# Kernel tuning notes

Measured on AMD Instinct MI355X. Metric: run time of the kernel, lower is better.

The kernel has to match this reference:

```python
import jax, jax.numpy as jnp
import numpy as np

EMBED = 1024
TOKLEN = 100
NLAYERS = 24
TOKDIM = 256
MLP = int(EMBED * 0.125)  # 128, hardcoded mlp_ratio=0.125
SEQ, BATCH = 4097, 8  # 4096 patch tokens + 1 cls token


def setup_inputs() -> dict:
    key = jax.random.key(0)
    ks = jax.random.split(key, 8)
    s = 0.02  # kaiming-like small init scale
    return {
        "x": jax.random.normal(ks[0], (SEQ, BATCH, EMBED), jnp.float32),
        "layer": 3,
        "A": jax.random.normal(ks[1], (1, TOKLEN, EMBED), jnp.float32) * s,
        "B": jax.random.normal(ks[2], (NLAYERS, EMBED, TOKDIM), jnp.float32) * s,
        "Wd": jax.random.normal(ks[3], (MLP, TOKDIM), jnp.float32) * s,
        "bd": jnp.zeros((MLP,), jnp.float32),
        "Wu": jax.random.normal(ks[4], (EMBED, MLP), jnp.float32) * s,
        "bu": jnp.zeros((EMBED,), jnp.float32),
        "Wt": jax.random.normal(ks[5], (EMBED, EMBED), jnp.float32) * s,
        "bt": jnp.zeros((EMBED,), jnp.float32),
        "Wf": jax.random.normal(ks[6], (EMBED, EMBED), jnp.float32) * s,
        "bf": jnp.zeros((EMBED,), jnp.float32),
        "scale": jnp.asarray(0.001, jnp.float32),
    }


def reference(x, layer, A, B, Wd, bd, Wu, bu, Wt, bt, Wf, bf, scale):
    # batch_first=False, has_cls_token=True, evp_feature=None (module defaults)
    cls_tok, body = x[:1], x[1:]              # [1,b,c], [n,b,c]
    # get_tokens(layer): tokens = A[0] @ up(gelu(down(B[layer])))
    Bl = B[layer]                              # [c, token_dim]
    fB = jax.nn.gelu(Bl @ Wd.T + bd, approximate=False) @ Wu.T + bu  # [c, c]
    tokens = A[0] @ fB                         # [m, c]
    # forward_delta_feat: cross-attention to the m=100 learned tokens
    attn = jax.nn.softmax(
        jnp.einsum("nbc,mc->nbm", body, tokens) * (EMBED ** -0.5), axis=-1
    )                                          # [n, b, m]
    tfeat = tokens @ Wt.T + bt                 # mlp_token2feat, [m, c]
    delta = jnp.einsum("nbm,mc->nbc", attn, tfeat)
    delta = (delta + body) @ Wf.T + bf         # mlp_delta_f
    out = body + delta * scale                 # scaled residual fuse
    return jnp.concatenate([cls_tok, out], axis=0)
```

## Files before the change

### kernel.cpp

```cpp
#include <hip/hip_runtime.h>
#include <stdint.h>

#define EMBED 1024
#define TOKLEN 100
#define TOKDIM 256
#define MLPD 128
#define KEXT 1152

typedef float f32x4 __attribute__((ext_vector_type(4)));
typedef __bf16 bf16x8 __attribute__((ext_vector_type(8)));

__device__ __forceinline__ unsigned short f2bf(float f) {
  unsigned int u = __float_as_uint(f);
  u += 0x7fffu + ((u >> 16) & 1);
  return (unsigned short)(u >> 16);
}
__device__ __forceinline__ float bf2f(unsigned short h) {
  return __uint_as_float(((unsigned int)h) << 16);
}
__device__ __forceinline__ void async16(const void* g, void* l) {
  __builtin_amdgcn_global_load_lds(
      (const __attribute__((address_space(1))) unsigned int*)g,
      (__attribute__((address_space(3))) unsigned int*)l, 16, 0, 0);
}



__global__ void k_gelu(const float* __restrict__ B, const int* __restrict__ layer,
                       const float* __restrict__ Wd, const float* __restrict__ bd,
                       float* __restrict__ G) {
  int idx = blockIdx.x * 256 + threadIdx.x;
  int c = idx >> 7, j = idx & 127;
  const float* bl = B + ((size_t)layer[0] * EMBED + c) * TOKDIM;
  const float* wd = Wd + (size_t)j * TOKDIM;
  float a0 = 0.f, a1 = 0.f, a2 = 0.f, a3 = 0.f;
  for (int k = 0; k < TOKDIM; k += 4) {
    float4 a = *(const float4*)(bl + k);
    float4 b = *(const float4*)(wd + k);
    a0 += a.x * b.x; a1 += a.y * b.y; a2 += a.z * b.z; a3 += a.w * b.w;
  }
  float v = a0 + a1 + a2 + a3 + bd[j];
  G[idx] = 0.5f * v * (1.f + erff(v * 0.70710678118654752440f));
}

__global__ void k_ag(const float* __restrict__ A, const float* __restrict__ G,
                     float* __restrict__ AG, float* __restrict__ asum) {
  int m = blockIdx.x, j = threadIdx.x;
  const float* a = A + (size_t)m * EMBED;
  float acc = 0.f, s = 0.f;
  for (int c = 0; c < EMBED; ++c) acc += a[c] * G[(size_t)c * MLPD + j];
  AG[(size_t)m * MLPD + j] = acc;
  for (int c = j; c < EMBED; c += 128) s += a[c];
  __shared__ float red[128];
  red[j] = s; __syncthreads();
  for (int w = 64; w > 0; w >>= 1) { if (j < w) red[j] += red[j + w]; __syncthreads(); }
  if (j == 0) asum[m] = red[0];
}

__global__ void k_tokens(const float* __restrict__ AG, const float* __restrict__ asum,
                         const float* __restrict__ Wu, const float* __restrict__ bu,
                         unsigned short* __restrict__ tokbf) {
  int m = blockIdx.x, t = threadIdx.x;
  if (m >= TOKLEN) {
    #pragma unroll
    for (int i = 0; i < 4; ++i) tokbf[(size_t)m * EMBED + t * 4 + i] = 0;
    return;
  }
  __shared__ float ag[MLPD];
  __shared__ float as_s;
  if (t < MLPD) ag[t] = AG[(size_t)m * MLPD + t];
  if (t == 0) as_s = asum[m];
  __syncthreads();
  #pragma unroll
  for (int i = 0; i < 4; ++i) {
    int e = t * 4 + i;
    const float* wu = Wu + (size_t)e * MLPD;
    float a0 = 0.f, a1 = 0.f, a2 = 0.f, a3 = 0.f;
    for (int j = 0; j < MLPD; j += 4) {
      float4 w = *(const float4*)(wu + j);
      a0 += w.x * ag[j]; a1 += w.y * ag[j + 1]; a2 += w.z * ag[j + 2]; a3 += w.w * ag[j + 3];
    }
    tokbf[(size_t)m * EMBED + e] = f2bf(a0 + a1 + a2 + a3 + as_s * bu[e]);
  }
}

__global__ void k_wfcvt(const float* __restrict__ Wf, unsigned short* __restrict__ Bt,
                        unsigned short* __restrict__ wfbf) {
  int e = blockIdx.x, t = threadIdx.x;
  float4 v = *(const float4*)(Wf + (size_t)e * EMBED + t * 4);
  uint2 u;
  u.x = (unsigned int)f2bf(v.x) | ((unsigned int)f2bf(v.y) << 16);
  u.y = (unsigned int)f2bf(v.z) | ((unsigned int)f2bf(v.w) << 16);
  *(uint2*)(Bt + (size_t)e * KEXT + t * 4) = u;
  *(uint2*)(wfbf + (size_t)e * EMBED + t * 4) = u;
  if (t < 28) Bt[(size_t)e * KEXT + 1124 + t] = 0;
}

__global__ void k_wtcvt(const float* __restrict__ Wt, unsigned short* __restrict__ wtbf) {
  int idx = blockIdx.x * 256 + threadIdx.x;
  float4 v = *(const float4*)(Wt + (size_t)idx * 4);
  uint2 u;
  u.x = (unsigned int)f2bf(v.x) | ((unsigned int)f2bf(v.y) << 16);
  u.y = (unsigned int)f2bf(v.z) | ((unsigned int)f2bf(v.w) << 16);
  *(uint2*)(wtbf + (size_t)idx * 4) = u;
}

__global__ void k_wfbt(const float* __restrict__ Wf, const float* __restrict__ bt,
                       float* __restrict__ wfbt) {
  int e = blockIdx.x, t = threadIdx.x;
  float4 w = *(const float4*)(Wf + (size_t)e * EMBED + t * 4);
  float4 b = *(const float4*)(bt + t * 4);
  __shared__ float red[256];
  red[t] = w.x * b.x + w.y * b.y + w.z * b.z + w.w * b.w;
  __syncthreads();
  for (int s = 128; s > 0; s >>= 1) { if (t < s) red[t] += red[t + s]; __syncthreads(); }
  if (t == 0) wfbt[e] = red[0];
}

__global__ void k_cls(const float* __restrict__ x, float* __restrict__ out) {
  int i = blockIdx.x * 256 + threadIdx.x;
  ((float4*)out)[i] = ((const float4*)x)[i];
}


__global__ void __launch_bounds__(256) k_tf1(const unsigned short* __restrict__ tokbf,
                                             const unsigned short* __restrict__ wtbf,
                                             unsigned short* __restrict__ tfeatbf) {
  __shared__ unsigned short As[128 * 64];
  __shared__ unsigned short Bs[128 * 64];
  const int tid = threadIdx.x;
  const int wave = tid >> 6, lane = tid & 63;
  const int l15 = lane & 15, quad = lane >> 4;
  const int srow = lane >> 3, schunk = lane & 7;
  const int col0 = blockIdx.x * 128;
  const int wr = (wave >> 1) * 64, wc = (wave & 1) * 64;

  f32x4 acc[4][4];
  const f32x4 zero = {0.f, 0.f, 0.f, 0.f};
  #pragma unroll
  for (int i = 0; i < 4; ++i)
    #pragma unroll
    for (int j = 0; j < 4; ++j) acc[i][j] = zero;

  for (int kt = 0; kt < 16; ++kt) {
    const int k0 = kt * 64;
    #pragma unroll
    for (int i = 0; i < 4; ++i) {
      const int r = i * 32 + wave * 8;
      async16(tokbf + (size_t)(r + srow) * EMBED + k0 + (schunk ^ srow) * 8, &As[r * 64]);
      async16(wtbf + (size_t)(col0 + r + srow) * EMBED + k0 + (schunk ^ srow) * 8, &Bs[r * 64]);
    }
    asm volatile("s_waitcnt vmcnt(0)" ::: "memory");
    __syncthreads();
    #pragma unroll
    for (int ks = 0; ks < 2; ++ks) {
      const int sw = ((ks * 4 + quad) ^ (l15 & 7)) * 8;
      bf16x8 a[4], b[4];
      #pragma unroll
      for (int i = 0; i < 4; ++i)
        a[i] = *(const bf16x8*)&As[(wr + i * 16 + l15) * 64 + sw];
      #pragma unroll
      for (int j = 0; j < 4; ++j)
        b[j] = *(const bf16x8*)&Bs[(wc + j * 16 + l15) * 64 + sw];
      #pragma unroll
      for (int i = 0; i < 4; ++i)
        #pragma unroll
        for (int j = 0; j < 4; ++j)
          acc[i][j] = __builtin_amdgcn_mfma_f32_16x16x32_bf16(a[i], b[j], acc[i][j], 0, 0, 0);
    }
    __syncthreads();
  }
  #pragma unroll
  for (int j = 0; j < 4; ++j) {
    const int e = col0 + wc + j * 16 + l15;
    #pragma unroll
    for (int i = 0; i < 4; ++i) {
      const int mb = wr + i * 16 + quad * 4;
      #pragma unroll
      for (int r = 0; r < 4; ++r)
        tfeatbf[(size_t)(mb + r) * EMBED + e] = f2bf(acc[i][j][r]);
    }
  }
}

__global__ void __launch_bounds__(256) k_tf2(const unsigned short* __restrict__ wfbf,
                                             const unsigned short* __restrict__ tfeatbf,
                                             const float* __restrict__ wfbt,
                                             unsigned short* __restrict__ Bt) {
  __shared__ unsigned short As[128 * 64];
  __shared__ unsigned short Bs[128 * 64];
  const int tid = threadIdx.x;
  const int wave = tid >> 6, lane = tid & 63;
  const int l15 = lane & 15, quad = lane >> 4;
  const int srow = lane >> 3, schunk = lane & 7;
  const int row0 = blockIdx.x * 128;
  const int wr = (wave >> 1) * 64, wc = (wave & 1) * 64;

  f32x4 acc[4][4];
  const f32x4 zero = {0.f, 0.f, 0.f, 0.f};
  #pragma unroll
  for (int i = 0; i < 4; ++i)
    #pragma unroll
    for (int j = 0; j < 4; ++j) acc[i][j] = zero;

  for (int kt = 0; kt < 16; ++kt) {
    const int k0 = kt * 64;
    #pragma unroll
    for (int i = 0; i < 4; ++i) {
      const int r = i * 32 + wave * 8;
      async16(wfbf + (size_t)(row0 + r + srow) * EMBED + k0 + (schunk ^ srow) * 8, &As[r * 64]);
      async16(tfeatbf + (size_t)(r + srow) * EMBED + k0 + (schunk ^ srow) * 8, &Bs[r * 64]);
    }
    asm volatile("s_waitcnt vmcnt(0)" ::: "memory");
    __syncthreads();
    #pragma unroll
    for (int ks = 0; ks < 2; ++ks) {
      const int sw = ((ks * 4 + quad) ^ (l15 & 7)) * 8;
      bf16x8 a[4], b[4];
      #pragma unroll
      for (int i = 0; i < 4; ++i)
        a[i] = *(const bf16x8*)&As[(wr + i * 16 + l15) * 64 + sw];
      #pragma unroll
      for (int j = 0; j < 4; ++j)
        b[j] = *(const bf16x8*)&Bs[(wc + j * 16 + l15) * 64 + sw];
      #pragma unroll
      for (int i = 0; i < 4; ++i)
        #pragma unroll
        for (int j = 0; j < 4; ++j)
          acc[i][j] = __builtin_amdgcn_mfma_f32_16x16x32_bf16(a[i], b[j], acc[i][j], 0, 0, 0);
    }
    __syncthreads();
  }
  #pragma unroll
  for (int j = 0; j < 4; ++j) {
    const int m = wc + j * 16 + l15;
    #pragma unroll
    for (int i = 0; i < 4; ++i) {
      const int eb = row0 + wr + i * 16 + quad * 4;
      #pragma unroll
      for (int r = 0; r < 4; ++r)
        Bt[(size_t)(eb + r) * KEXT + 1024 + m] = f2bf(acc[i][j][r] + wfbt[eb + r]);
    }
  }
}

__global__ void __launch_bounds__(256) k_attn(const float* __restrict__ x,
                                              const unsigned short* __restrict__ tokbf,
                                              unsigned short* __restrict__ Aext) {
  __shared__ unsigned short smem[128 * 72 + 128 * 64];
  unsigned short* As = smem;
  unsigned short* Ts = smem + 128 * 72;
  const int tid = threadIdx.x;
  const int wave = tid >> 6, lane = tid & 63;
  const int l15 = lane & 15, quad = lane >> 4;
  const int srow = lane >> 3, schunk = lane & 7;
  const int row0 = blockIdx.x * 128;
  const int trow = tid >> 1, thalf = tid & 1;
  const float* body = x + 8 * EMBED;

  f32x4 acc[2][8];
  const f32x4 zero = {0.f, 0.f, 0.f, 0.f};
  #pragma unroll
  for (int i = 0; i < 2; ++i)
    #pragma unroll
    for (int j = 0; j < 8; ++j) acc[i][j] = zero;

  for (int kt = 0; kt < 16; ++kt) {
    const int k0 = kt * 64;
    #pragma unroll
    for (int i = 0; i < 4; ++i) {
      const int r = i * 32 + wave * 8;
      async16(tokbf + (size_t)(r + srow) * EMBED + k0 + (schunk ^ srow) * 8, &Ts[r * 64]);
    }
    const float* gx = body + (size_t)(row0 + trow) * EMBED + k0 + thalf * 32;
    float4 v[8];
    #pragma unroll
    for (int q = 0; q < 8; ++q) v[q] = *(const float4*)(gx + q * 4);
    unsigned int pk[16];
    #pragma unroll
    for (int q = 0; q < 8; ++q) {
      pk[q * 2]     = (unsigned int)f2bf(v[q].x) | ((unsigned int)f2bf(v[q].y) << 16);
      pk[q * 2 + 1] = (unsigned int)f2bf(v[q].z) | ((unsigned int)f2bf(v[q].w) << 16);
    }
    unsigned int* lw = (unsigned int*)&As[trow * 72 + thalf * 32];
    unsigned int* gw = (unsigned int*)(Aext + (size_t)(row0 + trow) * KEXT + k0 + thalf * 32);
    #pragma unroll
    for (int q = 0; q < 4; ++q) {
      uint4 u; u.x = pk[q*4]; u.y = pk[q*4+1]; u.z = pk[q*4+2]; u.w = pk[q*4+3];
      ((uint4*)lw)[q] = u;
      ((uint4*)gw)[q] = u;
    }
    asm volatile("s_waitcnt vmcnt(0)" ::: "memory");
    __syncthreads();
    #pragma unroll
    for (int ks = 0; ks < 2; ++ks) {
      const int sw = ((ks * 4 + quad) ^ (l15 & 7)) * 8;
      bf16x8 a[2], b[8];
      #pragma unroll
      for (int i = 0; i < 2; ++i)
        a[i] = *(const bf16x8*)&As[(wave * 32 + i * 16 + l15) * 72 + ks * 32 + quad * 8];
      #pragma unroll
      for (int j = 0; j < 8; ++j)
        b[j] = *(const bf16x8*)&Ts[(j * 16 + l15) * 64 + sw];
      #pragma unroll
      for (int i = 0; i < 2; ++i)
        #pragma unroll
        for (int j = 0; j < 8; ++j)
          acc[i][j] = __builtin_amdgcn_mfma_f32_16x16x32_bf16(a[i], b[j], acc[i][j], 0, 0, 0);
    }
    __syncthreads();
  }

  unsigned short* Sc = smem;
  #pragma unroll
  for (int i = 0; i < 2; ++i) {
    const int rb = wave * 32 + i * 16 + quad * 4;
    #pragma unroll
    for (int j = 0; j < 8; ++j) {
      const int c = j * 16 + l15;
      #pragma unroll
      for (int r = 0; r < 4; ++r)
        Sc[(rb + r) * 128 + c] = f2bf(acc[i][j][r] * 0.03125f);
    }
  }
  __syncthreads();
  if (tid < 128) {
    unsigned short* row = Sc + tid * 128;
    float mx = -1e30f;
    for (int m = 0; m < TOKLEN; ++m) mx = fmaxf(mx, bf2f(row[m]));
    float s = 0.f;
    for (int m = 0; m < TOKLEN; ++m) s += __expf(bf2f(row[m]) - mx);
    float inv = 1.f / s;
    for (int m = 0; m < TOKLEN; ++m) row[m] = f2bf(__expf(bf2f(row[m]) - mx) * inv);
    for (int m = TOKLEN; m < 128; ++m) row[m] = 0;
  }
  __syncthreads();
  {
    const int r = tid >> 1, h = tid & 1;
    const uint4* src = (const uint4*)(Sc + r * 128 + h * 64);
    uint4* dst = (uint4*)(Aext + (size_t)(row0 + r) * KEXT + 1024 + h * 64);
    dst[0] = src[0]; dst[1] = src[1]; dst[2] = src[2]; dst[3] = src[3];
  }
}

__global__ void __launch_bounds__(256) k_main(const unsigned short* __restrict__ Aext,
                                              const unsigned short* __restrict__ Bt,
                                              const float* __restrict__ x,
                                              const float* __restrict__ bfv,
                                              const float* __restrict__ scale,
                                              float* __restrict__ out) {
  __shared__ unsigned short As[128 * 64];
  __shared__ unsigned short Bs[128 * 64];
  const int tid = threadIdx.x;
  const int wave = tid >> 6, lane = tid & 63;
  const int l15 = lane & 15, quad = lane >> 4;
  const int srow = lane >> 3, schunk = lane & 7;
  const int xcd = blockIdx.x & 7, slot = blockIdx.x >> 3;
  const int row0 = ((slot >> 3) * 8 + xcd) * 128;
  const int col0 = (slot & 7) * 128;
  const int wr = (wave >> 1) * 64, wc = (wave & 1) * 64;

  f32x4 acc[4][4];
  const f32x4 zero = {0.f, 0.f, 0.f, 0.f};
  #pragma unroll
  for (int i = 0; i < 4; ++i)
    #pragma unroll
    for (int j = 0; j < 4; ++j) acc[i][j] = zero;

  for (int kt = 0; kt < 18; ++kt) {
    const int k0 = kt * 64;
    #pragma unroll
    for (int i = 0; i < 4; ++i) {
      const int r = i * 32 + wave * 8;
      async16(Aext + (size_t)(row0 + r + srow) * KEXT + k0 + (schunk ^ srow) * 8, &As[r * 64]);
      async16(Bt   + (size_t)(col0 + r + srow) * KEXT + k0 + (schunk ^ srow) * 8, &Bs[r * 64]);
    }
    asm volatile("s_waitcnt vmcnt(0)" ::: "memory");
    __syncthreads();
    #pragma unroll
    for (int ks = 0; ks < 2; ++ks) {
      const int sw = ((ks * 4 + quad) ^ (l15 & 7)) * 8;
      bf16x8 a[4], b[4];
      #pragma unroll
      for (int i = 0; i < 4; ++i)
        a[i] = *(const bf16x8*)&As[(wr + i * 16 + l15) * 64 + sw];
      #pragma unroll
      for (int j = 0; j < 4; ++j)
        b[j] = *(const bf16x8*)&Bs[(wc + j * 16 + l15) * 64 + sw];
      #pragma unroll
      for (int i = 0; i < 4; ++i)
        #pragma unroll
        for (int j = 0; j < 4; ++j)
          acc[i][j] = __builtin_amdgcn_mfma_f32_16x16x32_bf16(a[i], b[j], acc[i][j], 0, 0, 0);
    }
    __syncthreads();
  }

  const float s = scale[0];
  #pragma unroll
  for (int j = 0; j < 4; ++j) {
    const int c = col0 + wc + j * 16 + l15;
    const float bfc = bfv[c];
    #pragma unroll
    for (int i = 0; i < 4; ++i) {
      const int rb = row0 + wr + i * 16 + quad * 4;
      #pragma unroll
      for (int r = 0; r < 4; ++r) {
        const size_t idx = (size_t)(rb + r + 8) * EMBED + c;
        out[idx] = x[idx] + (acc[i][j][r] + bfc) * s;
      }
    }
  }
}

extern "C" void kernel_launch(void* const* d_in, const int* in_sizes, int n_in,
                              void* d_out, int out_size, void* d_ws, size_t ws_size,
                              hipStream_t stream) {
  const float* x     = (const float*)d_in[0];
  const int*   layer = (const int*)d_in[1];
  const float* A     = (const float*)d_in[2];
  const float* B     = (const float*)d_in[3];
  const float* Wd    = (const float*)d_in[4];
  const float* bd    = (const float*)d_in[5];
  const float* Wu    = (const float*)d_in[6];
  const float* bu    = (const float*)d_in[7];
  const float* Wt    = (const float*)d_in[8];
  const float* bt    = (const float*)d_in[9];
  const float* Wf    = (const float*)d_in[10];
  const float* bf    = (const float*)d_in[11];
  const float* scale = (const float*)d_in[12];
  float* out = (float*)d_out;

  char* ws = (char*)d_ws;
  unsigned short* Aext    = (unsigned short*)(ws + 0);
  unsigned short* wtbf    = (unsigned short*)(ws + 0);
  unsigned short* wfbf    = (unsigned short*)(ws + 2097152);
  unsigned short* Bt_     = (unsigned short*)(ws + 75497472);
  unsigned short* tokbf   = (unsigned short*)(ws + 77856768);
  float*          G       = (float*)(ws + 78118912);
  float*          AG      = (float*)(ws + 78643200);
  float*          asum    = (float*)(ws + 78694400);
  float*          wfbt    = (float*)(ws + 78694912);
  unsigned short* tfeatbf = (unsigned short*)(ws + 78699008);

  k_gelu  <<<512, 256, 0, stream>>>(B, layer, Wd, bd, G);
  k_ag    <<<100, 128, 0, stream>>>(A, G, AG, asum);
  k_tokens<<<128, 256, 0, stream>>>(AG, asum, Wu, bu, tokbf);
  k_wfcvt <<<1024, 256, 0, stream>>>(Wf, Bt_, wfbf);
  k_wfbt  <<<1024, 256, 0, stream>>>(Wf, bt, wfbt);
  k_wtcvt <<<1024, 256, 0, stream>>>(Wt, wtbf);
  k_tf1   <<<8, 256, 0, stream>>>(tokbf, wtbf, tfeatbf);
  k_tf2   <<<8, 256, 0, stream>>>(wfbf, tfeatbf, wfbt, Bt_);
  k_cls   <<<8, 256, 0, stream>>>(x, out);
  k_attn  <<<256, 256, 0, stream>>>(x, tokbf, Aext);
  k_main  <<<2048, 256, 0, stream>>>(Aext, Bt_, x, bf, scale, out);
}
```

Measured before the change: 547.9 us.

## Double-buffer GEMM k-loops, fuse weight-prep kernels, do softmax in registers

Adds two-stage LDS double buffering to k_tf1, k_tf2, k_attn and k_main, so the loads for the next k-tile are issued before the MFMA work on the current tile. It also merges the three weight-conversion and bias kernels into a single k_wprep launch, and moves the attention softmax from a serial per-row loop over LDS into register-level wave shuffles. Doubling the shared memory per block may lower occupancy, especially for k_main. Each iteration still waits on vmcnt(0) after compute, which limits how much load and compute can overlap.

```diff
diff --git a/kernel.cpp b/kernel.cpp
--- a/kernel.cpp
+++ b/kernel.cpp
@@ -84,8 +84,10 @@
   }
 }
 
-__global__ void k_wfcvt(const float* __restrict__ Wf, unsigned short* __restrict__ Bt,
-                        unsigned short* __restrict__ wfbf) {
+__global__ void k_wprep(const float* __restrict__ Wf, const float* __restrict__ Wt,
+                        const float* __restrict__ bt,
+                        unsigned short* __restrict__ Bt, unsigned short* __restrict__ wfbf,
+                        unsigned short* __restrict__ wtbf, float* __restrict__ wfbt) {
   int e = blockIdx.x, t = threadIdx.x;
   float4 v = *(const float4*)(Wf + (size_t)e * EMBED + t * 4);
   uint2 u;
@@ -94,24 +96,14 @@
   *(uint2*)(Bt + (size_t)e * KEXT + t * 4) = u;
   *(uint2*)(wfbf + (size_t)e * EMBED + t * 4) = u;
   if (t < 28) Bt[(size_t)e * KEXT + 1124 + t] = 0;
-}
-
-__global__ void k_wtcvt(const float* __restrict__ Wt, unsigned short* __restrict__ wtbf) {
-  int idx = blockIdx.x * 256 + threadIdx.x;
-  float4 v = *(const float4*)(Wt + (size_t)idx * 4);
-  uint2 u;
-  u.x = (unsigned int)f2bf(v.x) | ((unsigned int)f2bf(v.y) << 16);
-  u.y = (unsigned int)f2bf(v.z) | ((unsigned int)f2bf(v.w) << 16);
-  *(uint2*)(wtbf + (size_t)idx * 4) = u;
-}
-
-__global__ void k_wfbt(const float* __restrict__ Wf, const float* __restrict__ bt,
-                       float* __restrict__ wfbt) {
-  int e = blockIdx.x, t = threadIdx.x;
-  float4 w = *(const float4*)(Wf + (size_t)e * EMBED + t * 4);
+  float4 w = *(const float4*)(Wt + (size_t)e * EMBED + t * 4);
+  uint2 u2;
+  u2.x = (unsigned int)f2bf(w.x) | ((unsigned int)f2bf(w.y) << 16);
+  u2.y = (unsigned int)f2bf(w.z) | ((unsigned int)f2bf(w.w) << 16);
+  *(uint2*)(wtbf + (size_t)e * EMBED + t * 4) = u2;
   float4 b = *(const float4*)(bt + t * 4);
   __shared__ float red[256];
-  red[t] = w.x * b.x + w.y * b.y + w.z * b.z + w.w * b.w;
+  red[t] = v.x * b.x + v.y * b.y + v.z * b.z + v.w * b.w;
   __syncthreads();
   for (int s = 128; s > 0; s >>= 1) { if (t < s) red[t] += red[t + s]; __syncthreads(); }
   if (t == 0) wfbt[e] = red[0];
@@ -126,8 +118,8 @@
 __global__ void __launch_bounds__(256) k_tf1(const unsigned short* __restrict__ tokbf,
                                              const unsigned short* __restrict__ wtbf,
                                              unsigned short* __restrict__ tfeatbf) {
-  __shared__ unsigned short As[128 * 64];
-  __shared__ unsigned short Bs[128 * 64];
+  __shared__ unsigned short As[2][128 * 64];
+  __shared__ unsigned short Bs[2][128 * 64];
   const int tid = threadIdx.x;
   const int wave = tid >> 6, lane = tid & 63;
   const int l15 = lane & 15, quad = lane >> 4;
@@ -142,33 +134,44 @@
     #pragma unroll
     for (int j = 0; j < 4; ++j) acc[i][j] = zero;
 
-  for (int kt = 0; kt < 16; ++kt) {
+  auto stage = [&](int buf, int kt) {
     const int k0 = kt * 64;
     #pragma unroll
     for (int i = 0; i < 4; ++i) {
       const int r = i * 32 + wave * 8;
-      async16(tokbf + (size_t)(r + srow) * EMBED + k0 + (schunk ^ srow) * 8, &As[r * 64]);
-      async16(wtbf + (size_t)(col0 + r + srow) * EMBED + k0 + (schunk ^ srow) * 8, &Bs[r * 64]);
-    }
-    asm volatile("s_waitcnt vmcnt(0)" ::: "memory");
-    __syncthreads();
+      async16(tokbf + (size_t)(r + srow) * EMBED + k0 + (schunk ^ srow) * 8, &As[buf][r * 64]);
+      async16(wtbf + (size_t)(col0 + r + srow) * EMBED + k0 + (schunk ^ srow) * 8, &Bs[buf][r * 64]);
+    }
+  };
+  auto compute = [&](int buf) {
     #pragma unroll
     for (int ks = 0; ks < 2; ++ks) {
       const int sw = ((ks * 4 + quad) ^ (l15 & 7)) * 8;
       bf16x8 a[4], b[4];
       #pragma unroll
       for (int i = 0; i < 4; ++i)
-        a[i] = *(const bf16x8*)&As[(wr + i * 16 + l15) * 64 + sw];
+        a[i] = *(const bf16x8*)&As[buf][(wr + i * 16 + l15) * 64 + sw];
       #pragma unroll
       for (int j = 0; j < 4; ++j)
-        b[j] = *(const bf16x8*)&Bs[(wc + j * 16 + l15) * 64 + sw];
+        b[j] = *(const bf16x8*)&Bs[buf][(wc + j * 16 + l15) * 64 + sw];
       #pragma unroll
       for (int i = 0; i < 4; ++i)
         #pragma unroll
         for (int j = 0; j < 4; ++j)
           acc[i][j] = __builtin_amdgcn_mfma_f32_16x16x32_bf16(a[i], b[j], acc[i][j], 0, 0, 0);
     }
+  };
+
+  stage(0, 0);
+  asm volatile("s_waitcnt vmcnt(0)" ::: "memory");
+  __syncthreads();
+  int cur = 0;
+  for (int kt = 0; kt < 16; ++kt) {
+    if (kt < 15) stage(cur ^ 1, kt + 1);
+    compute(cur);
+    asm volatile("s_waitcnt vmcnt(0)" ::: "memory");
     __syncthreads();
+    cur ^= 1;
   }
   #pragma unroll
   for (int j = 0; j < 4; ++j) {
@@ -187,8 +190,8 @@
                                              const unsigned short* __restrict__ tfeatbf,
                                              const float* __restrict__ wfbt,
                                              unsigned short* __restrict__ Bt) {
-  __shared__ unsigned short As[128 * 64];
-  __shared__ unsigned short Bs[128 * 64];
+  __shared__ unsigned short As[2][128 * 64];
+  __shared__ unsigned short Bs[2][128 * 64];
   const int tid = threadIdx.x;
   const int wave = tid >> 6, lane = tid & 63;
   const int l15 = lane & 15, quad = lane >> 4;
@@ -203,33 +206,44 @@
     #pragma unroll
     for (int j = 0; j < 4; ++j) acc[i][j] = zero;
 
-  for (int kt = 0; kt < 16; ++kt) {
+  auto stage = [&](int buf, int kt) {
     const int k0 = kt * 64;
     #pragma unroll
     for (int i = 0; i < 4; ++i) {
       const int r = i * 32 + wave * 8;
-      async16(wfbf + (size_t)(row0 + r + srow) * EMBED + k0 + (schunk ^ srow) * 8, &As[r * 64]);
-      async16(tfeatbf + (size_t)(r + srow) * EMBED + k0 + (schunk ^ srow) * 8, &Bs[r * 64]);
-    }
-    asm volatile("s_waitcnt vmcnt(0)" ::: "memory");
-    __syncthreads();
+      async16(wfbf + (size_t)(row0 + r + srow) * EMBED + k0 + (schunk ^ srow) * 8, &As[buf][r * 64]);
+      async16(tfeatbf + (size_t)(r + srow) * EMBED + k0 + (schunk ^ srow) * 8, &Bs[buf][r * 64]);
+    }
+  };
+  auto compute = [&](int buf) {
     #pragma unroll
     for (int ks = 0; ks < 2; ++ks) {
       const int sw = ((ks * 4 + quad) ^ (l15 & 7)) * 8;
       bf16x8 a[4], b[4];
       #pragma unroll
       for (int i = 0; i < 4; ++i)
-        a[i] = *(const bf16x8*)&As[(wr + i * 16 + l15) * 64 + sw];
+        a[i] = *(const bf16x8*)&As[buf][(wr + i * 16 + l15) * 64 + sw];
       #pragma unroll
       for (int j = 0; j < 4; ++j)
-        b[j] = *(const bf16x8*)&Bs[(wc + j * 16 + l15) * 64 + sw];
+        b[j] = *(const bf16x8*)&Bs[buf][(wc + j * 16 + l15) * 64 + sw];
       #pragma unroll
       for (int i = 0; i < 4; ++i)
         #pragma unroll
         for (int j = 0; j < 4; ++j)
           acc[i][j] = __builtin_amdgcn_mfma_f32_16x16x32_bf16(a[i], b[j], acc[i][j], 0, 0, 0);
     }
+  };
+
+  stage(0, 0);
+  asm volatile("s_waitcnt vmcnt(0)" ::: "memory");
+  __syncthreads();
+  int cur = 0;
+  for (int kt = 0; kt < 16; ++kt) {
+    if (kt < 15) stage(cur ^ 1, kt + 1);
+    compute(cur);
+    asm volatile("s_waitcnt vmcnt(0)" ::: "memory");
     __syncthreads();
+    cur ^= 1;
   }
   #pragma unroll
   for (int j = 0; j < 4; ++j) {
@@ -247,9 +261,7 @@
 __global__ void __launch_bounds__(256) k_attn(const float* __restrict__ x,
                                               const unsigned short* __restrict__ tokbf,
                                               unsigned short* __restrict__ Aext) {
-  __shared__ unsigned short smem[128 * 72 + 128 * 64];
-  unsigned short* As = smem;
-  unsigned short* Ts = smem + 128 * 72;
+  __shared__ __align__(16) unsigned short smem[2 * 128 * 72 + 2 * 128 * 64];
   const int tid = threadIdx.x;
   const int wave = tid >> 6, lane = tid & 63;
   const int l15 = lane & 15, quad = lane >> 4;
@@ -257,6 +269,7 @@
   const int row0 = blockIdx.x * 128;
   const int trow = tid >> 1, thalf = tid & 1;
   const float* body = x + 8 * EMBED;
+  const float* gxbase = body + (size_t)(row0 + trow) * EMBED + thalf * 32;
 
   f32x4 acc[2][8];
   const f32x4 zero = {0.f, 0.f, 0.f, 0.f};
@@ -265,17 +278,24 @@
     #pragma unroll
     for (int j = 0; j < 8; ++j) acc[i][j] = zero;
 
-  for (int kt = 0; kt < 16; ++kt) {
+  float4 v[8];
+
+  auto regload = [&](int kt) {
+    const float* gx = gxbase + kt * 64;
+    #pragma unroll
+    for (int q = 0; q < 8; ++q) v[q] = *(const float4*)(gx + q * 4);
+  };
+  auto tsstage = [&](int buf, int kt) {
+    unsigned short* Ts = smem + 2 * 128 * 72 + buf * (128 * 64);
     const int k0 = kt * 64;
     #pragma unroll
     for (int i = 0; i < 4; ++i) {
       const int r = i * 32 + wave * 8;
       async16(tokbf + (size_t)(r + srow) * EMBED + k0 + (schunk ^ srow) * 8, &Ts[r * 64]);
     }
-    const float* gx = body + (size_t)(row0 + trow) * EMBED + k0 + thalf * 32;
-    float4 v[8];
-    #pragma unroll
-    for (int q = 0; q < 8; ++q) v[q] = *(const float4*)(gx + q * 4);
+  };
+  auto convwrite = [&](int buf, int kt) {
+    unsigned short* As = smem + buf * (128 * 72);
     unsigned int pk[16];
     #pragma unroll
     for (int q = 0; q < 8; ++q) {
@@ -283,15 +303,17 @@
       pk[q * 2 + 1] = (unsigned int)f2bf(v[q].z) | ((unsigned int)f2bf(v[q].w) << 16);
     }
     unsigned int* lw = (unsigned int*)&As[trow * 72 + thalf * 32];
-    unsigned int* gw = (unsigned int*)(Aext + (size_t)(row0 + trow) * KEXT + k0 + thalf * 32);
+    unsigned int* gw = (unsigned int*)(Aext + (size_t)(row0 + trow) * KEXT + kt * 64 + thalf * 32);
     #pragma unroll
     for (int q = 0; q < 4; ++q) {
       uint4 u; u.x = pk[q*4]; u.y = pk[q*4+1]; u.z = pk[q*4+2]; u.w = pk[q*4+3];
       ((uint4*)lw)[q] = u;
       ((uint4*)gw)[q] = u;
     }
-    asm volatile("s_waitcnt vmcnt(0)" ::: "memory");
-    __syncthreads();
+  };
+  auto compute = [&](int buf) {
+    unsigned short* As = smem + buf * (128 * 72);
+    unsigned short* Ts = smem + 2 * 128 * 72 + buf * (128 * 64);
     #pragma unroll
     for (int ks = 0; ks < 2; ++ks) {
       const int sw = ((ks * 4 + quad) ^ (l15 & 7)) * 8;
@@ -308,31 +330,55 @@
         for (int j = 0; j < 8; ++j)
           acc[i][j] = __builtin_amdgcn_mfma_f32_16x16x32_bf16(a[i], b[j], acc[i][j], 0, 0, 0);
     }
+  };
+
+  regload(0); tsstage(0, 0);
+  asm volatile("s_waitcnt vmcnt(0)" ::: "memory");
+  convwrite(0, 0);
+  __syncthreads();
+  int cur = 0;
+  for (int kt = 0; kt < 16; ++kt) {
+    if (kt < 15) { regload(kt + 1); tsstage(cur ^ 1, kt + 1); }
+    compute(cur);
+    if (kt < 15) {
+      asm volatile("s_waitcnt vmcnt(0)" ::: "memory");
+      convwrite(cur ^ 1, kt + 1);
+    }
     __syncthreads();
+    cur ^= 1;
   }
 
   unsigned short* Sc = smem;
   #pragma unroll
   for (int i = 0; i < 2; ++i) {
-    const int rb = wave * 32 + i * 16 + quad * 4;
-    #pragma unroll
-    for (int j = 0; j < 8; ++j) {
-      const int c = j * 16 + l15;
-      #pragma unroll
-      for (int r = 0; r < 4; ++r)
-        Sc[(rb + r) * 128 + c] = f2bf(acc[i][j][r] * 0.03125f);
-    }
-  }
-  __syncthreads();
-  if (tid < 128) {
-    unsigned short* row = Sc + tid * 128;
-    float mx = -1e30f;
-    for (int m = 0; m < TOKLEN; ++m) mx = fmaxf(mx, bf2f(row[m]));
-    float s = 0.f;
-    for (int m = 0; m < TOKLEN; ++m) s += __expf(bf2f(row[m]) - mx);
-    float inv = 1.f / s;
-    for (int m = 0; m < TOKLEN; ++m) row[m] = f2bf(__expf(bf2f(row[m]) - mx) * inv);
-    for (int m = TOKLEN; m < 128; ++m) row[m] = 0;
+    #pragma unroll
+    for (int r = 0; r < 4; ++r) {
+      float mx = -1e30f;
+      #pragma unroll
+      for (int j = 0; j < 8; ++j) {
+        const int c = j * 16 + l15;
+        const float vv = acc[i][j][r] * 0.03125f;
+        if (c < TOKLEN) mx = fmaxf(mx, vv);
+      }
+      #pragma unroll
+      for (int d = 1; d < 16; d <<= 1) mx = fmaxf(mx, __shfl_xor(mx, d));
+      float sm = 0.f;
+      #pragma unroll
+      for (int j = 0; j < 8; ++j) {
+        const int c = j * 16 + l15;
+        if (c < TOKLEN) sm += __expf(acc[i][j][r] * 0.03125f - mx);
+      }
+      #pragma unroll
+      for (int d = 1; d < 16; d <<= 1) sm += __shfl_xor(sm, d);
+      const float inv = 1.f / sm;
+      const int row = wave * 32 + i * 16 + quad * 4 + r;
+      #pragma unroll
+      for (int j = 0; j < 8; ++j) {
+        const int c = j * 16 + l15;
+        const float p = (c < TOKLEN) ? __expf(acc[i][j][r] * 0.03125f - mx) * inv : 0.f;
+        Sc[row * 128 + c] = f2bf(p);
+      }
+    }
   }
   __syncthreads();
   {
@@ -349,8 +395,8 @@
                                               const float* __restrict__ bfv,
                                               const float* __restrict__ scale,
                                               float* __restrict__ out) {
-  __shared__ unsigned short As[128 * 64];
-  __shared__ unsigned short Bs[128 * 64];
+  __shared__ unsigned short As[2][128 * 64];
+  __shared__ unsigned short Bs[2][128 * 64];
   const int tid = threadIdx.x;
   const int wave = tid >> 6, lane = tid & 63;
   const int l15 = lane & 15, quad = lane >> 4;
@@ -367,33 +413,44 @@
     #pragma unroll
     for (int j = 0; j < 4; ++j) acc[i][j] = zero;
 
-  for (int kt = 0; kt < 18; ++kt) {
+  auto stage = [&](int buf, int kt) {
     const int k0 = kt * 64;
     #pragma unroll
     for (int i = 0; i < 4; ++i) {
       const int r = i * 32 + wave * 8;
-      async16(Aext + (size_t)(row0 + r + srow) * KEXT + k0 + (schunk ^ srow) * 8, &As[r * 64]);
-      async16(Bt   + (size_t)(col0 + r + srow) * KEXT + k0 + (schunk ^ srow) * 8, &Bs[r * 64]);
-    }
-    asm volatile("s_waitcnt vmcnt(0)" ::: "memory");
-    __syncthreads();
+      async16(Aext + (size_t)(row0 + r + srow) * KEXT + k0 + (schunk ^ srow) * 8, &As[buf][r * 64]);
+      async16(Bt   + (size_t)(col0 + r + srow) * KEXT + k0 + (schunk ^ srow) * 8, &Bs[buf][r * 64]);
+    }
+  };
+  auto compute = [&](int buf) {
     #pragma unroll
     for (int ks = 0; ks < 2; ++ks) {
       const int sw = ((ks * 4 + quad) ^ (l15 & 7)) * 8;
       bf16x8 a[4], b[4];
       #pragma unroll
       for (int i = 0; i < 4; ++i)
-        a[i] = *(const bf16x8*)&As[(wr + i * 16 + l15) * 64 + sw];
+        a[i] = *(const bf16x8*)&As[buf][(wr + i * 16 + l15) * 64 + sw];
       #pragma unroll
       for (int j = 0; j < 4; ++j)
-        b[j] = *(const bf16x8*)&Bs[(wc + j * 16 + l15) * 64 + sw];
+        b[j] = *(const bf16x8*)&Bs[buf][(wc + j * 16 + l15) * 64 + sw];
       #pragma unroll
       for (int i = 0; i < 4; ++i)
         #pragma unroll
         for (int j = 0; j < 4; ++j)
           acc[i][j] = __builtin_amdgcn_mfma_f32_16x16x32_bf16(a[i], b[j], acc[i][j], 0, 0, 0);
     }
+  };
+
+  stage(0, 0);
+  asm volatile("s_waitcnt vmcnt(0)" ::: "memory");
+  __syncthreads();
+  int cur = 0;
+  for (int kt = 0; kt < 18; ++kt) {
+    if (kt < 17) stage(cur ^ 1, kt + 1);
+    compute(cur);
+    asm volatile("s_waitcnt vmcnt(0)" ::: "memory");
     __syncthreads();
+    cur ^= 1;
   }
 
   const float s = scale[0];
@@ -446,9 +503,7 @@
   k_gelu  <<<512, 256, 0, stream>>>(B, layer, Wd, bd, G);
   k_ag    <<<100, 128, 0, stream>>>(A, G, AG, asum);
   k_tokens<<<128, 256, 0, stream>>>(AG, asum, Wu, bu, tokbf);
-  k_wfcvt <<<1024, 256, 0, stream>>>(Wf, Bt_, wfbf);
-  k_wfbt  <<<1024, 256, 0, stream>>>(Wf, bt, wfbt);
-  k_wtcvt <<<1024, 256, 0, stream>>>(Wt, wtbf);
+  k_wprep <<<1024, 256, 0, stream>>>(Wf, Wt, bt, Bt_, wfbf, wtbf, wfbt);
   k_tf1   <<<8, 256, 0, stream>>>(tokbf, wtbf, tfeatbf);
   k_tf2   <<<8, 256, 0, stream>>>(wfbf, tfeatbf, wfbt, Bt_);
   k_cls   <<<8, 256, 0, stream>>>(x, out);
```

After: 538.8 us. About the same (-1.6%).
